# Kernel optimization log

Hardware: AMD Instinct MI355X
Metric: run time of the kernel (lower is better)

## Reference

```python
import jax, jax.numpy as jnp
import numpy as np
import math

NFFT = 2048; HOP = 512; BINS = NFFT // 2 + 1  # 1025
HEADS = 2; D = 2 * BINS; DFF = 4 * D          # 2050, 8200
BATCH = 4; LEN = 441000


def _stft(x, window):
    # replicates torch.stft(center=True, pad_mode='reflect', onesided=True)
    pad = NFFT // 2
    xp = jnp.pad(x, ((0, 0), (pad, pad)), mode='reflect')
    n_frames = 1 + (xp.shape[-1] - NFFT) // HOP
    idx = jnp.arange(n_frames)[:, None] * HOP + jnp.arange(NFFT)[None, :]
    frames = xp[:, idx] * window                      # (N, T, NFFT)
    return jnp.fft.rfft(frames, axis=-1).transpose(0, 2, 1)  # (N, BINS, T)


def _istft(spec, window, length):
    # replicates torch.istft(center=True, length=length)
    frames = jnp.fft.irfft(spec.transpose(0, 2, 1), n=NFFT, axis=-1) * window  # (N,T,NFFT)
    T = frames.shape[1]
    out_len = NFFT + HOP * (T - 1)
    idx = jnp.arange(T)[:, None] * HOP + jnp.arange(NFFT)[None, :]
    out = jnp.zeros((frames.shape[0], out_len), frames.dtype).at[:, idx].add(frames)
    wsq = jnp.zeros((out_len,), window.dtype).at[idx].add(window ** 2)
    out = out / jnp.where(wsq > 1e-11, wsq, 1.0)
    pad = NFFT // 2
    return out[:, pad:pad + length]


def _pos_enc(d, T):
    pos = jnp.arange(T, dtype=jnp.float32)[:, None]
    div = jnp.exp(jnp.arange(0, d, 2, dtype=jnp.float32) * (-math.log(10000.0) / d))
    pe = jnp.zeros((T, d), jnp.float32)
    pe = pe.at[:, 0::2].set(jnp.sin(pos * div)).at[:, 1::2].set(jnp.cos(pos * div))
    return pe[None]


def _ln(x, g, b):
    m = x.mean(-1, keepdims=True)
    v = x.var(-1, keepdims=True)
    return (x - m) / jnp.sqrt(v + 1e-5) * g + b


def _clin(r, i, Wr, br, Wi, bi):
    # (Lr(r) - Li(i), Lr(i) + Li(r))
    return (r @ Wr.T + br) - (i @ Wi.T + bi), (i @ Wr.T + br) + (r @ Wi.T + bi)


def _cconv1x1(r, i, wr, br, wi, bi):
    # 1x1 grouped conv with in=out=2, groups=2 -> per-channel scale+bias
    s = lambda x, w, b: x * w[None, :, None, None] + b[None, :, None, None]
    return s(r, wr, br) - s(i, wi, bi), s(i, wr, br) + s(r, wi, bi)


def _cattn(r, i, Win, bin_, Wo, bo):
    # 8 shared-weight MHA calls; only 4 distinct (Q,K) softmax maps, each
    # applied to two V tensors (the fusion opportunity). Eval mode: no dropout.
    B, S, _ = r.shape
    hd = D // HEADS
    Wq, Wk, Wv = Win[:D], Win[D:2 * D], Win[2 * D:]
    bq, bk, bv = bin_[:D], bin_[D:2 * D], bin_[2 * D:]
    proj = lambda x, W, b: (x @ W.T + b).reshape(B, S, HEADS, hd).transpose(0, 2, 1, 3)
    qr, qi = proj(r, Wq, bq), proj(i, Wq, bq)
    kr, ki = proj(r, Wk, bk), proj(i, Wk, bk)
    vr, vi = proj(r, Wv, bv), proj(i, Wv, bv)
    scale = 1.0 / math.sqrt(hd)
    A = lambda q, k: jax.nn.softmax(jnp.einsum('bhqd,bhkd->bhqk', q, k) * scale, axis=-1)
    Arr, Ari, Air, Aii = A(qr, kr), A(qr, ki), A(qi, kr), A(qi, ki)
    ap = lambda Aw, v: jnp.einsum('bhqk,bhkd->bhqd', Aw, v)
    out_r = ap(Arr, vr) + ap(Ari, vi) - ap(Air, vi) - ap(Aii, vr)
    out_i = ap(Arr, vi) + ap(Ari, vr) + ap(Air, vr) - ap(Aii, vi)
    merge = lambda o: o.transpose(0, 2, 1, 3).reshape(B, S, D)
    # out_proj bias coefficients: real part (+1+1-1-1)=0, imag part (+1+1+1-1)=2
    return merge(out_r) @ Wo.T, merge(out_i) @ Wo.T + 2.0 * bo


def reference(mix, window, c1wr, c1br, c1wi, c1bi, c2wr, c2br, c2wi, c2bi,
              attn_in_w, attn_in_b, attn_out_w, attn_out_b,
              l1wr, l1br, l1wi, l1bi, l2wr, l2br, l2wi, l2bi,
              n1_gr, n1_br, n1_gi, n1_bi, n2_gr, n2_br, n2_gi, n2_bi):
    B, C, L = mix.shape
    spec = _stft(mix.reshape(-1, L), window)      # (B*2, BINS, T)
    T = spec.shape[-1]
    spec = spec.reshape(-1, 2, BINS, T)           # (B, 2, BINS, T)
    real, imag = jnp.real(spec), jnp.imag(spec)
    nr, ni = _cconv1x1(real, imag, c1wr, c1br, c1wi, c1bi)
    nr = nr.transpose(0, 3, 2, 1).reshape(B, T, D)   # torch .transpose(1,3).reshape
    ni = ni.transpose(0, 3, 2, 1).reshape(B, T, D)
    pe = _pos_enc(D, T)
    nr, ni = nr + pe, ni + pe
    nr, ni = _cattn(nr, ni, attn_in_w, attn_in_b, attn_out_w, attn_out_b)
    nr, ni = _ln(nr, n1_gr, n1_br), _ln(ni, n1_gi, n1_bi)   # dropout = identity (eval)
    hr, hi = _clin(nr, ni, l1wr, l1br, l1wi, l1bi)
    hr, hi = jax.nn.relu(hr), jax.nn.relu(hi)
    hr, hi = _clin(hr, hi, l2wr, l2br, l2wi, l2bi)
    nr, ni = _ln(hr, n2_gr, n2_br), _ln(hi, n2_gi, n2_bi)
    nr = nr.reshape(B, T, BINS, 2).transpose(0, 3, 2, 1)    # (B,2,BINS,T)
    ni = ni.reshape(B, T, BINS, 2).transpose(0, 3, 2, 1)
    mr, mi = _cconv1x1(nr, ni, c2wr, c2br, c2wi, c2bi)
    real = real * jax.nn.sigmoid(mr)
    imag = imag * jax.nn.sigmoid(mi)
    spec2 = (real + 1j * imag).reshape(-1, BINS, T)
    estim = _istft(spec2, window, L).reshape(-1, 2, L)
    return estim, jnp.stack((jnp.real(spec2), jnp.imag(spec2)), axis=-1)


def setup_inputs() -> dict:
    key = jax.random.key(0)
    ks = jax.random.split(key, 32)
    W = 0.02
    rn = lambda k, shp, s=W: jax.random.normal(k, shp, jnp.float32) * s
    hann = 0.5 * (1.0 - jnp.cos(2.0 * jnp.pi * jnp.arange(NFFT, dtype=jnp.float32) / NFFT))
    inp = {
        'mix': rn(ks[0], (BATCH, 2, LEN), 1.0),
        'window': hann,
        'c1wr': rn(ks[1], (2,), 0.5), 'c1br': rn(ks[2], (2,), 0.1),
        'c1wi': rn(ks[3], (2,), 0.5), 'c1bi': rn(ks[4], (2,), 0.1),
        'c2wr': rn(ks[5], (2,), 0.5), 'c2br': rn(ks[6], (2,), 0.1),
        'c2wi': rn(ks[7], (2,), 0.5), 'c2bi': rn(ks[8], (2,), 0.1),
        'attn_in_w': rn(ks[9], (3 * D, D)), 'attn_in_b': rn(ks[10], (3 * D,)),
        'attn_out_w': rn(ks[11], (D, D)), 'attn_out_b': rn(ks[12], (D,)),
        'l1wr': rn(ks[13], (DFF, D)), 'l1br': rn(ks[14], (DFF,)),
        'l1wi': rn(ks[15], (DFF, D)), 'l1bi': rn(ks[16], (DFF,)),
        'l2wr': rn(ks[17], (D, DFF)), 'l2br': rn(ks[18], (D,)),
        'l2wi': rn(ks[19], (D, DFF)), 'l2bi': rn(ks[20], (D,)),
        'n1_gr': jnp.ones((D,), jnp.float32), 'n1_br': jnp.zeros((D,), jnp.float32),
        'n1_gi': jnp.ones((D,), jnp.float32), 'n1_bi': jnp.zeros((D,), jnp.float32),
        'n2_gr': jnp.ones((D,), jnp.float32), 'n2_br': jnp.zeros((D,), jnp.float32),
        'n2_gi': jnp.ones((D,), jnp.float32), 'n2_bi': jnp.zeros((D,), jnp.float32),
    }
    return inp
```

## Files before the change

### kernel.cpp

```cpp
#include <hip/hip_runtime.h>
#include <hip/hip_bf16.h>
#include <math.h>

#ifndef M_PIf
#define M_PIf 3.14159265358979323846f
#endif

static constexpr int kNFFT = 2048;
static constexpr int kHOP  = 512;
static constexpr int kBINS = 1025;
static constexpr int kT    = 862;
static constexpr int kL    = 441000;
static constexpr int kB    = 4;
static constexpr int kNSIG = 8;
static constexpr int kD    = 2050;
static constexpr int kHD   = 1025;
static constexpr int kDFF  = 8200;
static constexpr int kBS   = kB * kT;
static constexpr float kAttnScale = 0.031234752377721214f;
static constexpr long kS2  = (long)kT * kT;
static constexpr int kTP   = 864;
static constexpr long kS2P = (long)kT * kTP;
static constexpr int kDP   = 2056;
static constexpr int kHDP  = 1032;
static constexpr int kHDP2 = 1056;
static constexpr int kQKr  = 3488;
static constexpr int kWr   = 1152;
static constexpr int kNH   = 4104;
static constexpr int kDP2  = 2080;
static constexpr int kNHP  = 4128;
static constexpr int kMP   = 3456;
static constexpr int kW1R  = 4352;
static constexpr int kW2R  = 2304;

using bf16 = __hip_bfloat16;
typedef __attribute__((ext_vector_type(4))) float f32x4;
typedef __attribute__((ext_vector_type(8))) short bf16x8;

__device__ __forceinline__ float ldf(const float* p, long i) { return p[i]; }
__device__ __forceinline__ float ldf(const bf16* p, long i) {
  return __bfloat162float(p[i]);
}
__device__ __forceinline__ void sto(float* p, long i, float v) { p[i] = v; }
__device__ __forceinline__ void sto(bf16* p, long i, float v) {
  p[i] = __float2bfloat16(v);
}
__device__ __forceinline__ void load16(const float* src, bf16* dst) {
#pragma unroll
  for (int e = 0; e < 16; ++e) dst[e] = __float2bfloat16(src[e]);
}
__device__ __forceinline__ void load16(const bf16* src, bf16* dst) {
  *(bf16x8*)(dst)     = *(const bf16x8*)(src);
  *(bf16x8*)(dst + 8) = *(const bf16x8*)(src + 8);
}

__device__ __forceinline__ void glds16(const bf16* g, bf16* l) {
  __builtin_amdgcn_global_load_lds(
      (const __attribute__((address_space(1))) unsigned int*)g,
      (__attribute__((address_space(3))) unsigned int*)l, 16, 0, 0);
}

__device__ __forceinline__ void xcd_swizzle(int& bx, int& by) {
  int nwg = gridDim.x * gridDim.y;
  int orig = by * gridDim.x + bx;
  int qq = nwg >> 3, rr = nwg & 7;
  int xcd = orig & 7, loc = orig >> 3;
  int wg = (xcd < rr ? xcd * (qq + 1) : rr * (qq + 1) + (xcd - rr) * qq) + loc;
  bx = wg % gridDim.x;
  by = wg / gridDim.x;
}

__device__ __forceinline__ void pipe_wait8() {
  asm volatile("s_waitcnt vmcnt(8)" ::: "memory");
  __builtin_amdgcn_sched_barrier(0);
  __builtin_amdgcn_s_barrier();
  __builtin_amdgcn_sched_barrier(0);
}
__device__ __forceinline__ void pipe_wait0() {
  asm volatile("s_waitcnt vmcnt(0)" ::: "memory");
  __builtin_amdgcn_sched_barrier(0);
  __builtin_amdgcn_s_barrier();
  __builtin_amdgcn_sched_barrier(0);
}
__device__ __forceinline__ void pipe_readdone() {
  __builtin_amdgcn_sched_barrier(0);
  __builtin_amdgcn_s_barrier();
  __builtin_amdgcn_sched_barrier(0);
}

template <typename T>
__device__ __forceinline__ void stage_row16(const T* S, int grow, int glim,
                                            int lda, int k0sk, int K,
                                            bf16* dst) {
  bf16 tmp[16];
  if (grow < glim && k0sk + 16 <= K) {
    load16(S + (long)grow * lda + k0sk, tmp);
  } else {
#pragma unroll
    for (int e = 0; e < 16; ++e) {
      int gk = k0sk + e;
      tmp[e] = __float2bfloat16(
          (grow < glim && gk < K) ? ldf(S, (long)grow * lda + gk) : 0.f);
    }
  }
  *(bf16x8*)(dst)     = *(bf16x8*)&tmp[0];
  *(bf16x8*)(dst + 8) = *(bf16x8*)&tmp[8];
}

__global__ void k_twiddle(float2* __restrict__ tw) {
  int m = blockIdx.x * 256 + threadIdx.x;
  if (m < 1024) {
    float s, c;
    sincosf(M_PIf * (float)m / 1024.f, &s, &c);
    tw[m] = make_float2(c, s);
  }
}

__device__ __forceinline__ void fft2048_lds(float*& sr, float*& si,
                                            float* dr, float* di, int tid,
                                            float dir,
                                            const float2* __restrict__ tw) {
  int s = 0;
  for (int Ns = 1; Ns < 2048; Ns <<= 1, ++s) {
#pragma unroll
    for (int q = 0; q < 4; ++q) {
      int j = tid + q * 256;
      int base = j & (Ns - 1);
      int grp = j >> s;
      float2 t = tw[base << (10 - s)];
      float c = t.x, sn = dir * t.y;
      float ar = sr[j],        ai = si[j];
      float br = sr[j + 1024], bi = si[j + 1024];
      float tbr = br * c - bi * sn;
      float tbi = br * sn + bi * c;
      int o = (grp << (s + 1)) + base;
      dr[o]      = ar + tbr;  di[o]      = ai + tbi;
      dr[o + Ns] = ar - tbr;  di[o + Ns] = ai - tbi;
    }
    __syncthreads();
    float* t0 = sr; sr = dr; dr = t0;
    float* t1 = si; si = di; di = t1;
  }
}

__global__ __launch_bounds__(256) void k_stft(const float* __restrict__ mix,
                                              const float* __restrict__ win,
                                              const float2* __restrict__ tw,
                                              float* __restrict__ spec) {
  __shared__ float b0r[2048], b0i[2048], b1r[2048], b1i[2048];
  int t = blockIdx.x, sig = blockIdx.y, tid = threadIdx.x;
  const float* x = mix + (long)sig * kL;
  for (int i = tid; i < 2048; i += 256) {
    int src = t * kHOP + i - 1024;
    if (src < 0) src = -src;
    if (src >= kL) src = 2 * kL - 2 - src;
    b0r[i] = x[src] * win[i];
    b0i[i] = 0.f;
  }
  __syncthreads();
  float* sr = b0r; float* si = b0i;
  fft2048_lds(sr, si, b1r, b1i, tid, -1.f, tw);
  for (int k = tid; k < kBINS; k += 256) {
    long o = ((long)sig * kBINS + k) * kT + t;
    spec[o * 2]     = sr[k];
    spec[o * 2 + 1] = si[k];
  }
}

__global__ __launch_bounds__(256) void k_istft(const float* __restrict__ spec,
                                               const float* __restrict__ win,
// ... 13 lines not shown
  }
  __syncthreads();
  float* sr = b0r; float* si = b0i;
  fft2048_lds(sr, si, b1r, b1i, tid, +1.f, tw);
  const float scale = 1.f / 2048.f;
  float* fo = frames + ((long)sig * kT + t) * 2048;
  for (int n = tid; n < 2048; n += 256) fo[n] = sr[n] * scale * win[n];
}

__global__ void k_gather(const float* __restrict__ frames,
                         const float* __restrict__ win,
                         float* __restrict__ out0) {
  long idx = (long)blockIdx.x * 256 + threadIdx.x;
  long total = (long)kNSIG * kL;
  if (idx >= total) return;
  int sig = (int)(idx / kL);
  int l = (int)(idx % kL);
  int j = l + 1024;
  int tmax = j >> 9; if (tmax > kT - 1) tmax = kT - 1;
  int v = j - 1536;
  int tmin = v > 0 ? (v >> 9) : 0;
  float acc = 0.f, w2 = 0.f;
  for (int t = tmin; t <= tmax; ++t) {
    int n = j - (t << 9);
    float w = win[n];
    acc += frames[((long)sig * kT + t) * 2048 + n];
    w2 = fmaf(w, w, w2);
  }
  out0[idx] = acc / (w2 > 1e-11f ? w2 : 1.f);
}

__global__ void k_conv1_pe(const float* __restrict__ spec,
                           const float* __restrict__ c1wr, const float* __restrict__ c1br,
                           const float* __restrict__ c1wi, const float* __restrict__ c1bi,
                           bf16* __restrict__ xrh, bf16* __restrict__ xrl,
                           bf16* __restrict__ xih, bf16* __restrict__ xil) {
  long idx = (long)blockIdx.x * 256 + threadIdx.x;
  long total = (long)kB * 2 * kBINS * kT;
  if (idx >= total) return;
  int t = (int)(idx % kT);
  long r0 = idx / kT;
  int bin = (int)(r0 % kBINS);
  long r1 = r0 / kBINS;
  int ch = (int)(r1 % 2);
  int b = (int)(r1 / 2);
  float re = spec[idx * 2], im = spec[idx * 2 + 1];
  float wr = c1wr[ch], br = c1br[ch], wi = c1wi[ch], bi = c1bi[ch];
  float nr = (re * wr + br) - (im * wi + bi);
  float ni = (im * wr + br) + (re * wi + bi);
  int d = bin * 2 + ch;
  int k = d >> 1;
  float dv = expf((float)k * (-9.210340371976184f / 1025.0f));
  float arg = (float)t * dv;
  float pe = (d & 1) ? cosf(arg) : sinf(arg);
  long ro = ((long)(b * kT + t)) * kDP2 + d;
  float vr = nr + pe, vi = ni + pe;
  bf16 hr = __float2bfloat16(vr);
  bf16 hi = __float2bfloat16(vi);
  xrh[ro] = hr; xrl[ro] = __float2bfloat16(vr - __bfloat162float(hr));
  xih[ro] = hi; xil[ro] = __float2bfloat16(vi - __bfloat162float(hi));
}

__global__ void k_cvt2(const float* __restrict__ src, bf16* __restrict__ dst,
                       long total, int ldd, int srows, int scols, int lds) {
  long idx = (long)blockIdx.x * 256 + threadIdx.x;
  if (idx >= total) return;
  int r = (int)(idx / ldd), c = (int)(idx % ldd);
  float v = (r < srows && c < scols) ? src[(long)r * lds + c] : 0.f;
  dst[idx] = __float2bfloat16(v);
}

__global__ void k_cvt2s(const float* __restrict__ src, bf16* __restrict__ dh,
                        bf16* __restrict__ dl, long total, int ldd, int srows,
                        int scols, int lds) {
  long idx = (long)blockIdx.x * 256 + threadIdx.x;
  if (idx >= total) return;
  int r = (int)(idx / ldd), c = (int)(idx % ldd);
  float v = (r < srows && c < scols) ? src[(long)r * lds + c] : 0.f;
  bf16 h = __float2bfloat16(v);
  dh[idx] = h;
  dl[idx] = __float2bfloat16(v - __bfloat162float(h));
}

template <typename TA, typename TC>
__global__ __launch_bounds__(256) void k_mfma2(
    const TA* __restrict__ A1, const TA* __restrict__ A2,
    const bf16* __restrict__ B, TC* __restrict__ C1, TC* __restrict__ C2,
    const float* __restrict__ bias, float bs1, float bs2,
    int M, int N, int K, int lda, int ldb, int ldc) {
  __shared__ __align__(16) bf16 As1[128][40];
  __shared__ __align__(16) bf16 As2[128][40];
  __shared__ __align__(16) bf16 Bs[128][40];
  int tid = threadIdx.x;
  int bm = blockIdx.y * 128, bn = blockIdx.x * 128;
  int lane = tid & 63, w = tid >> 6;
  int wr = (w >> 1) * 64, wc = (w & 1) * 64;
  int fr = lane & 15, fq = lane >> 4;
  f32x4 ac1[4][4] = {}, ac2[4][4] = {};
  int sr = tid >> 1, sk = (tid & 1) * 16;
  for (int k0 = 0; k0 < K; k0 += 32) {
    stage_row16(A1, bm + sr, M, lda, k0 + sk, K, &As1[sr][sk]);
    stage_row16(A2, bm + sr, M, lda, k0 + sk, K, &As2[sr][sk]);
    stage_row16(B,  bn + sr, N, ldb, k0 + sk, K, &Bs[sr][sk]);
    __syncthreads();
    bf16x8 a1[4], a2[4], b[4];
#pragma unroll
    for (int i = 0; i < 4; ++i) {
      a1[i] = *(const bf16x8*)&As1[wr + i * 16 + fr][fq * 8];
      a2[i] = *(const bf16x8*)&As2[wr + i * 16 + fr][fq * 8];
      b[i]  = *(const bf16x8*)&Bs[wc + i * 16 + fr][fq * 8];
    }
#pragma unroll
    for (int i = 0; i < 4; ++i)
#pragma unroll
      for (int j = 0; j < 4; ++j) {
        ac1[i][j] = __builtin_amdgcn_mfma_f32_16x16x32_bf16(a1[i], b[j], ac1[i][j], 0, 0, 0);
        ac2[i][j] = __builtin_amdgcn_mfma_f32_16x16x32_bf16(a2[i], b[j], ac2[i][j], 0, 0, 0);
      }
    __syncthreads();
  }
#pragma unroll
  for (int i = 0; i < 4; ++i)
#pragma unroll
    for (int j = 0; j < 4; ++j) {
      int gn = bn + wc + j * 16 + fr;
      if (gn >= N) continue;
      float bv = bias ? bias[gn] : 0.f;
#pragma unroll
      for (int r = 0; r < 4; ++r) {
        int gm = bm + wr + i * 16 + fq * 4 + r;
        if (gm >= M) continue;
        long co = (long)gm * ldc + gn;
        sto(C1, co, ac1[i][j][r] + bs1 * bv);
        sto(C2, co, ac2[i][j][r] + bs2 * bv);
      }
    }
}

__global__ __launch_bounds__(256) void k_gemm3s(
    const bf16* __restrict__ Ah, const bf16* __restrict__ Al,
    const bf16* __restrict__ Bh, const bf16* __restrict__ Bl,
    bf16* __restrict__ Ch, bf16* __restrict__ Cl,
    const float* __restrict__ bias,
    int M, int N, int K, int lda, int ldb, int ldc) {
  __shared__ __align__(16) bf16 Sah[2][128][32];
  __shared__ __align__(16) bf16 Sal[2][128][32];
  __shared__ __align__(16) bf16 Sbh[2][128][32];
  __shared__ __align__(16) bf16 Sbl[2][128][32];
  int bx = blockIdx.x, by = blockIdx.y;
  xcd_swizzle(bx, by);
  int bm = by * 128, bn = bx * 128;
  int tid = threadIdx.x;
  int lane = tid & 63, w = tid >> 6;
  int wr = (w >> 1) * 64, wc = (w & 1) * 64;
  int fr = lane & 15, fq = lane >> 4;
  f32x4 acc[4][4] = {};
  int srow = w * 32 + (lane >> 2);
  int scol = (lane & 3) * 8;
  const bf16* pAh[2]; const bf16* pAl[2];
  const bf16* pBh[2]; const bf16* pBl[2];
#pragma unroll
  for (int c = 0; c < 2; ++c) {
    long ga = (long)(bm + srow + c * 16) * lda + scol;
    long gb = (long)(bn + srow + c * 16) * ldb + scol;
    pAh[c] = Ah + ga; pAl[c] = Al + ga;
    pBh[c] = Bh + gb; pBl[c] = Bl + gb;
  }
  int nt = K >> 5;
#pragma unroll
  for (int c = 0; c < 2; ++c) {
    int lb = w * 1024 + c * 512;
    glds16(pAh[c], &Sah[0][0][0] + lb);
    glds16(pAl[c], &Sal[0][0][0] + lb);
    glds16(pBh[c], &Sbh[0][0][0] + lb);
    glds16(pBl[c], &Sbl[0][0][0] + lb);
  }
  if (nt > 1) {
#pragma unroll
    for (int c = 0; c < 2; ++c) {
      int lb = 4096 + w * 1024 + c * 512;
      glds16(pAh[c] + 32, &Sah[0][0][0] + lb);
      glds16(pAl[c] + 32, &Sal[0][0][0] + lb);
      glds16(pBh[c] + 32, &Sbh[0][0][0] + lb);
      glds16(pBl[c] + 32, &Sbl[0][0][0] + lb);
    }
  }
  long koff = 64;
  for (int t = 0; t < nt; ++t) {
    int p = t & 1;
    if (t + 1 < nt) pipe_wait8(); else pipe_wait0();
    bf16x8 ah[4], al[4], bh[4], bl[4];
#pragma unroll
    for (int i = 0; i < 4; ++i) {
      ah[i] = *(const bf16x8*)&Sah[p][wr + i * 16 + fr][fq * 8];
      al[i] = *(const bf16x8*)&Sal[p][wr + i * 16 + fr][fq * 8];
      bh[i] = *(const bf16x8*)&Sbh[p][wc + i * 16 + fr][fq * 8];
      bl[i] = *(const bf16x8*)&Sbl[p][wc + i * 16 + fr][fq * 8];
    }
#pragma unroll
    for (int i = 0; i < 4; ++i)
#pragma unroll
      for (int j = 0; j < 4; ++j) {
        acc[i][j] = __builtin_amdgcn_mfma_f32_16x16x32_bf16(ah[i], bh[j], acc[i][j], 0, 0, 0);
        acc[i][j] = __builtin_amdgcn_mfma_f32_16x16x32_bf16(ah[i], bl[j], acc[i][j], 0, 0, 0);
        acc[i][j] = __builtin_amdgcn_mfma_f32_16x16x32_bf16(al[i], bh[j], acc[i][j], 0, 0, 0);
      }
    pipe_readdone();
    if (t + 2 < nt) {
      int pb = p * 4096;
#pragma unroll
      for (int c = 0; c < 2; ++c) {
        int lb = pb + w * 1024 + c * 512;
        glds16(pAh[c] + koff, &Sah[0][0][0] + lb);
        glds16(pAl[c] + koff, &Sal[0][0][0] + lb);
        glds16(pBh[c] + koff, &Sbh[0][0][0] + lb);
        glds16(pBl[c] + koff, &Sbl[0][0][0] + lb);
      }
      koff += 32;
    }
  }
#pragma unroll
  for (int i = 0; i < 4; ++i)
#pragma unroll
    for (int j = 0; j < 4; ++j) {
      int gn = bn + wc + j * 16 + fr;
      if (gn >= N) continue;
      float bv = bias[gn];
#pragma unroll
      for (int r = 0; r < 4; ++r) {
        int gm = bm + wr + i * 16 + fq * 4 + r;
        if (gm >= M) continue;
        long co = (long)gm * ldc + gn;
        float v = acc[i][j][r] + bv;
        bf16 h = __float2bfloat16(v);
        Ch[co] = h;
        Cl[co] = __float2bfloat16(v - __bfloat162float(h));
      }
    }
}

__global__ __launch_bounds__(256) void k_qkt3(
    const bf16* __restrict__ Qrh, const bf16* __restrict__ Qrl,
    const bf16* __restrict__ Qih, const bf16* __restrict__ Qil,
    const bf16* __restrict__ Krh, const bf16* __restrict__ Krl,
    const bf16* __restrict__ Kih, const bf16* __restrict__ Kil,
    float* __restrict__ S, int bp) {
  __shared__ __align__(16) bf16 Sqh[2][128][32];
  __shared__ __align__(16) bf16 Sql[2][128][32];
  __shared__ __align__(16) bf16 Skh[2][128][32];
  __shared__ __align__(16) bf16 Skl[2][128][32];
  int bl = blockIdx.z >> 2, c = blockIdx.z & 3;
  int b = bp * 2 + bl;
  long roff = (long)b * kT * kHDP2;
  const bf16* qh = ((c >> 1) ? Qih : Qrh) + roff;
  const bf16* ql = ((c >> 1) ? Qil : Qrl) + roff;
  const bf16* kh = ((c & 1) ? Kih : Krh) + roff;
  const bf16* kl = ((c & 1) ? Kil : Krl) + roff;
  float* So = S + ((long)bl * 4 + c) * kS2;
  int bx = blockIdx.x, by = blockIdx.y;
  xcd_swizzle(bx, by);
  int bm = by * 128, bn = bx * 128;
  int tid = threadIdx.x;
  int lane = tid & 63, w = tid >> 6;
  int wr = (w >> 1) * 64, wc = (w & 1) * 64;
  int fr = lane & 15, fq = lane >> 4;
  f32x4 acc[4][4] = {};
  int srow = w * 32 + (lane >> 2);
  int scol = (lane & 3) * 8;
  const bf16* pQh[2]; const bf16* pQl[2];
  const bf16* pKh[2]; const bf16* pKl[2];
#pragma unroll
  for (int cc = 0; cc < 2; ++cc) {
    long ga = (long)(bm + srow + cc * 16) * kHDP2 + scol;
    long gb = (long)(bn + srow + cc * 16) * kHDP2 + scol;
    pQh[cc] = qh + ga; pQl[cc] = ql + ga;
    pKh[cc] = kh + gb; pKl[cc] = kl + gb;
  }
  int nt = kHDP2 >> 5;
#pragma unroll
  for (int cc = 0; cc < 2; ++cc) {
    int lb = w * 1024 + cc * 512;
    glds16(pQh[cc], &Sqh[0][0][0] + lb);
    glds16(pQl[cc], &Sql[0][0][0] + lb);
    glds16(pKh[cc], &Skh[0][0][0] + lb);
    glds16(pKl[cc], &Skl[0][0][0] + lb);
  }
  if (nt > 1) {
#pragma unroll
    for (int cc = 0; cc < 2; ++cc) {
      int lb = 4096 + w * 1024 + cc * 512;
      glds16(pQh[cc] + 32, &Sqh[0][0][0] + lb);
      glds16(pQl[cc] + 32, &Sql[0][0][0] + lb);
      glds16(pKh[cc] + 32, &Skh[0][0][0] + lb);
      glds16(pKl[cc] + 32, &Skl[0][0][0] + lb);
    }
  }
  long koff = 64;
  for (int t = 0; t < nt; ++t) {
    int p = t & 1;
    if (t + 1 < nt) pipe_wait8(); else pipe_wait0();
    bf16x8 ah[4], al[4], bh[4], blv[4];
#pragma unroll
    for (int i = 0; i < 4; ++i) {
      ah[i]  = *(const bf16x8*)&Sqh[p][wr + i * 16 + fr][fq * 8];
      al[i]  = *(const bf16x8*)&Sql[p][wr + i * 16 + fr][fq * 8];
      bh[i]  = *(const bf16x8*)&Skh[p][wc + i * 16 + fr][fq * 8];
      blv[i] = *(const bf16x8*)&Skl[p][wc + i * 16 + fr][fq * 8];
    }
#pragma unroll
    for (int i = 0; i < 4; ++i)
#pragma unroll
      for (int j = 0; j < 4; ++j) {
        acc[i][j] = __builtin_amdgcn_mfma_f32_16x16x32_bf16(ah[i], bh[j],  acc[i][j], 0, 0, 0);
        acc[i][j] = __builtin_amdgcn_mfma_f32_16x16x32_bf16(ah[i], blv[j], acc[i][j], 0, 0, 0);
        acc[i][j] = __builtin_amdgcn_mfma_f32_16x16x32_bf16(al[i], bh[j],  acc[i][j], 0, 0, 0);
      }
    pipe_readdone();
    if (t + 2 < nt) {
      int pb = p * 4096;
#pragma unroll
      for (int cc = 0; cc < 2; ++cc) {
        int lb = pb + w * 1024 + cc * 512;
        glds16(pQh[cc] + koff, &Sqh[0][0][0] + lb);
        glds16(pQl[cc] + koff, &Sql[0][0][0] + lb);
        glds16(pKh[cc] + koff, &Skh[0][0][0] + lb);
        glds16(pKl[cc] + koff, &Skl[0][0][0] + lb);
      }
      koff += 32;
    }
  }
#pragma unroll
  for (int i = 0; i < 4; ++i)
#pragma unroll
    for (int j = 0; j < 4; ++j) {
      int gn = bn + wc + j * 16 + fr;
      if (gn >= kT) continue;
#pragma unroll
      for (int r = 0; r < 4; ++r) {
        int gm = bm + wr + i * 16 + fq * 4 + r;
        if (gm >= kT) continue;
        So[(long)gm * kT + gn] = acc[i][j][r];
      }
    }
}

template <typename TC>
__global__ __launch_bounds__(512) void k_cgemm(
    const bf16* __restrict__ Ar, const bf16* __restrict__ Ai,
    const bf16* __restrict__ Br, const bf16* __restrict__ Bi,
    TC* __restrict__ Cr, TC* __restrict__ Ci,
    const float* __restrict__ biasR, const float* __restrict__ biasI,
    float bscale, int accum, int relu, int Nreal,
    int M, int N, int K, int lda, int ldb, int ldc) {
  __shared__ __align__(16) bf16 Asr[128][32];
  __shared__ __align__(16) bf16 Asi[128][32];
  __shared__ __align__(16) bf16 Bsr[256][32];
  __shared__ __align__(16) bf16 Bsi[256][32];
  int bx = blockIdx.x, by = blockIdx.y;
  xcd_swizzle(bx, by);
  int bm = by * 128, bn = bx * 256;
  int tid = threadIdx.x;
  int lane = tid & 63, w = tid >> 6;
  int wr = (w >> 2) * 64, wc = (w & 3) * 64;
  int fr = lane & 15, fq = lane >> 4;
  f32x4 acR[4][4] = {}, acI[4][4] = {};
  int srow = w * 16 + (lane >> 2);
  int scol = (lane & 3) * 8;
  const bf16* pAr = Ar + (long)(bm + srow) * lda + scol;
  const bf16* pAi = Ai + (long)(bm + srow) * lda + scol;
  const bf16* pBr[2];
  const bf16* pBi[2];
#pragma unroll
  for (int c = 0; c < 2; ++c) {
    long gb = (long)(bn + c * 128 + srow) * ldb + scol;
    pBr[c] = Br + gb;
    pBi[c] = Bi + gb;
  }
  const short ks = (short)0x8000;
  const bf16x8 sgn = {ks, ks, ks, ks, ks, ks, ks, ks};
  for (int k0 = 0; k0 < K; k0 += 32) {
    glds16(pAr + k0, &Asr[0][0] + w * 512);
    glds16(pAi + k0, &Asi[0][0] + w * 512);
#pragma unroll
    for (int c = 0; c < 2; ++c) {
      int lb = c * 4096 + w * 512;
      glds16(pBr[c] + k0, &Bsr[0][0] + lb);
      glds16(pBi[c] + k0, &Bsi[0][0] + lb);
    }
    __syncthreads();
    bf16x8 ar[4], ai[4], nai[4];
#pragma unroll
    for (int i = 0; i < 4; ++i) {
      ar[i] = *(const bf16x8*)&Asr[wr + i * 16 + fr][fq * 8];
      ai[i] = *(const bf16x8*)&Asi[wr + i * 16 + fr][fq * 8];
      nai[i] = ai[i] ^ sgn;
    }
#pragma unroll
    for (int j = 0; j < 4; ++j) {
      bf16x8 br = *(const bf16x8*)&Bsr[wc + j * 16 + fr][fq * 8];
      bf16x8 bi = *(const bf16x8*)&Bsi[wc + j * 16 + fr][fq * 8];
#pragma unroll
      for (int i = 0; i < 4; ++i) {
        acR[i][j] = __builtin_amdgcn_mfma_f32_16x16x32_bf16(ar[i],  br, acR[i][j], 0, 0, 0);
        acR[i][j] = __builtin_amdgcn_mfma_f32_16x16x32_bf16(nai[i], bi, acR[i][j], 0, 0, 0);
        acI[i][j] = __builtin_amdgcn_mfma_f32_16x16x32_bf16(ai[i],  br, acI[i][j], 0, 0, 0);
        acI[i][j] = __builtin_amdgcn_mfma_f32_16x16x32_bf16(ar[i],  bi, acI[i][j], 0, 0, 0);
      }
    }
    __syncthreads();
  }
#pragma unroll
  for (int i = 0; i < 4; ++i)
// ... 173 lines not shown
  float* x = X + row * d;
  int tid = threadIdx.x;
  float s = 0.f, s2 = 0.f;
  for (int i = tid; i < d; i += 256) {
    float v = x[i];
    s += v;
    s2 = fmaf(v, v, s2);
  }
  __shared__ float rs[4], rs2[4];
  for (int o = 32; o > 0; o >>= 1) {
    s += __shfl_down(s, o);
    s2 += __shfl_down(s2, o);
  }
  int lane = tid & 63, w = tid >> 6;
  if (lane == 0) { rs[w] = s; rs2[w] = s2; }
  __syncthreads();
  float st = rs[0] + rs[1] + rs[2] + rs[3];
  float s2t = rs2[0] + rs2[1] + rs2[2] + rs2[3];
  float m = st / d;
  float var = s2t / d - m * m;
  float inv = rsqrtf(var + 1e-5f);
  for (int i = tid; i < d; i += 256) x[i] = (x[i] - m) * inv * g[i] + b[i];
}

__global__ void k_mask(const float* __restrict__ gr_, const float* __restrict__ gi_,
                       const float* __restrict__ c2wr, const float* __restrict__ c2br,
                       const float* __restrict__ c2wi, const float* __restrict__ c2bi,
                       float* __restrict__ spec) {
  long idx = (long)blockIdx.x * 256 + threadIdx.x;
  long total = (long)kB * 2 * kBINS * kT;
  if (idx >= total) return;
  int t = (int)(idx % kT);
  long r0 = idx / kT;
  int bin = (int)(r0 % kBINS);
  long r1 = r0 / kBINS;
  int ch = (int)(r1 % 2);
  int b = (int)(r1 / 2);
  long ro = ((long)(b * kT + t)) * kD + (bin * 2 + ch);
  float gr = gr_[ro], gi = gi_[ro];
  float wr = c2wr[ch], br = c2br[ch], wi = c2wi[ch], bi = c2bi[ch];
  float mr = (gr * wr + br) - (gi * wi + bi);
  float mi = (gi * wr + br) + (gr * wi + bi);
  float re = spec[idx * 2], im = spec[idx * 2 + 1];
  spec[idx * 2]     = re / (1.f + expf(-mr));
  spec[idx * 2 + 1] = im / (1.f + expf(-mi));
}

extern "C" void kernel_launch(void* const* d_in, const int* in_sizes, int n_in,
                              void* d_out, int out_size, void* d_ws, size_t ws_size,
                              hipStream_t stream) {
  const float* mix        = (const float*)d_in[0];
  const float* window     = (const float*)d_in[1];
  const float* c1wr       = (const float*)d_in[2];
  const float* c1br       = (const float*)d_in[3];
  const float* c1wi       = (const float*)d_in[4];
  const float* c1bi       = (const float*)d_in[5];
  const float* c2wr       = (const float*)d_in[6];
  const float* c2br       = (const float*)d_in[7];
  const float* c2wi       = (const float*)d_in[8];
  const float* c2bi       = (const float*)d_in[9];
  const float* attn_in_w  = (const float*)d_in[10];
  const float* attn_in_b  = (const float*)d_in[11];
  const float* attn_out_w = (const float*)d_in[12];
  const float* attn_out_b = (const float*)d_in[13];
  const float* l1wr       = (const float*)d_in[14];
  const float* l1br       = (const float*)d_in[15];
  const float* l1wi       = (const float*)d_in[16];
  const float* l1bi       = (const float*)d_in[17];
  const float* l2wr       = (const float*)d_in[18];
  const float* l2br       = (const float*)d_in[19];
  const float* l2wi       = (const float*)d_in[20];
  const float* l2bi       = (const float*)d_in[21];
  const float* n1_gr      = (const float*)d_in[22];
  const float* n1_br      = (const float*)d_in[23];
  const float* n1_gi      = (const float*)d_in[24];
  const float* n1_bi      = (const float*)d_in[25];
  const float* n2_gr      = (const float*)d_in[26];
  const float* n2_br      = (const float*)d_in[27];
  const float* n2_gi      = (const float*)d_in[28];
  const float* n2_bi      = (const float*)d_in[29];

  constexpr long eX    = (long)kMP * kDP2;
  constexpr long eQK2  = (long)kQKr * kHDP2;
  constexpr long eAout = (long)kBS * kDP;
  constexpr long eV    = (long)kBS * kHDP;
  constexpr long eWp   = (long)kWr * kDP2;
  constexpr long eHidp = (long)kMP * kNHP;
  constexpr long eW1p  = (long)kW1R * kDP2;
  constexpr long eW2p  = (long)kW2R * kNHP;

  constexpr size_t oX    = 0;
  constexpr size_t oQK   = oX + 4 * eX * 2;
  constexpr size_t oAout = oQK + 8 * eQK2 * 2;
  constexpr size_t oV    = oAout + 2 * eAout * 2;
  constexpr size_t oW    = oV + 2 * eV * 2;
  constexpr size_t oP    = oW + 5 * eWp * 2;
  constexpr size_t oTW   = oP + 3 * kS2P * 2;
  constexpr size_t kNeed = 188922816;
  static_assert(oTW + 8192 <= kNeed, "tw overflow");
  constexpr size_t oSS = oW;
  static_assert(oSS + 8 * kS2 * 4 <= oP, "sS overflow");
  static_assert(2 * (long)kBS * kD * 4 <= (long)oQK, "xr/xi overlay");
  static_assert((long)kD * kDP * 2 <= (long)(oW - oV), "Wob overlay");
  constexpr size_t oAb  = oQK;
  constexpr size_t oWF  = oAb + 2 * eX * 2;
  constexpr size_t oHid = oWF + 2 * eW2p * 2;
  static_assert(2 * eW1p * 2 <= 2 * eW2p * 2, "W slot sized by W2");
  static_assert(oHid + 2 * eHidp * 2 <= oTW, "hid overflow");
  static_assert((long)kNSIG * kT * 2048 * 4 <= (long)(oTW - oAb), "frames");

  char* wsb = (char*)d_ws;
  if (ws_size < kNeed) return;

  bf16*  Xrh = (bf16*)(wsb + oX);
  bf16*  Xrl = Xrh + eX;
  bf16*  Xih = Xrl + eX;
  bf16*  Xil = Xih + eX;
  bf16*  Qrh = (bf16*)(wsb + oQK);
  bf16*  Qrl = Qrh + eQK2;
  bf16*  Qih = Qrl + eQK2;
  bf16*  Qil = Qih + eQK2;
  bf16*  Krh = Qil + eQK2;
  bf16*  Krl = Krh + eQK2;
  bf16*  Kih = Krl + eQK2;
  bf16*  Kil = Kih + eQK2;
  bf16*  aoutR = (bf16*)(wsb + oAout);
  bf16*  aoutI = aoutR + eAout;
  bf16*  Vr = (bf16*)(wsb + oV);
  bf16*  Vi = Vr + eV;
  bf16*  Wqh = (bf16*)(wsb + oW);
  bf16*  Wql = Wqh + eWp;
  bf16*  Wkh = Wql + eWp;
  bf16*  Wkl = Wkh + eWp;
  bf16*  Wvh = Wkl + eWp;
  float* sS = (float*)(wsb + oSS);
  bf16*  Pbuf = (bf16*)(wsb + oP);
  bf16*  Wob = (bf16*)(wsb + oV);
  float* xr = (float*)(wsb + oX);
  float* xi = xr + (long)kBS * kD;
  bf16*  AbR = (bf16*)(wsb + oAb);
  bf16*  AbI = AbR + eX;
  bf16*  w1rH = (bf16*)(wsb + oWF);
  bf16*  w1iH = w1rH + eW1p;
  bf16*  w2rH = (bf16*)(wsb + oWF);
  bf16*  w2iH = w2rH + eW2p;
  bf16*  hidR = (bf16*)(wsb + oHid);
  bf16*  hidI = hidR + eHidp;
  float* frames = (float*)(wsb + oAb);
  float2* tw = (float2*)(wsb + oTW);

  float* out0 = (float*)d_out;
  float* spec = out0 + (long)kNSIG * kL;

  auto cvt2 = [&](const float* src, bf16* dst, int dstRows, int ldd,
                  int srows, int scols, int lds) {
    long total = (long)dstRows * ldd;
    k_cvt2<<<(int)((total + 255) / 256), 256, 0, stream>>>(src, dst, total,
                                                           ldd, srows, scols,
                                                           lds);
  };
  auto cvt2s = [&](const float* src, bf16* dh, bf16* dl, int dstRows, int ldd,
                   int srows, int scols, int lds) {
    long total = (long)dstRows * ldd;
    k_cvt2s<<<(int)((total + 255) / 256), 256, 0, stream>>>(
        src, dh, dl, total, ldd, srows, scols, lds);
  };

  hipMemsetAsync(d_ws, 0, kNeed, stream);
  k_twiddle<<<4, 256, 0, stream>>>(tw);

  k_stft<<<dim3(kT, kNSIG), 256, 0, stream>>>(mix, window, tw, spec);

  long nct = (long)kB * 2 * kBINS * kT;
  k_conv1_pe<<<(nct + 255) / 256, 256, 0, stream>>>(spec, c1wr, c1br, c1wi,
                                                    c1bi, Xrh, Xrl, Xih, Xil);

  for (int h = 0; h < 2; ++h) {
    const float* Wq = attn_in_w + (long)(h * kHD) * kD;
    const float* Wk = attn_in_w + (long)(kD + h * kHD) * kD;
    const float* Wv = attn_in_w + (long)(2 * kD + h * kHD) * kD;
    const float* bq = attn_in_b + h * kHD;
    const float* bk = attn_in_b + kD + h * kHD;
    const float* bv = attn_in_b + 2 * kD + h * kHD;
    cvt2s(Wq, Wqh, Wql, kWr, kDP2, kHD, kD, kD);
    cvt2s(Wk, Wkh, Wkl, kWr, kDP2, kHD, kD, kD);
    cvt2(Wv, Wvh, kWr, kDP2, kHD, kD, kD);
    k_mfma2<bf16, bf16><<<dim3(9, 27), 256, 0, stream>>>(
        Xrh, Xih, Wvh, Vr, Vi, bv, 1.f, 1.f, kBS, kHD, kD, kDP2, kDP2, kHDP);
    k_gemm3s<<<dim3(9, 27), 256, 0, stream>>>(
        Xrh, Xrl, Wqh, Wql, Qrh, Qrl, bq, kBS, kHD, kDP2, kDP2, kDP2, kHDP2);
    k_gemm3s<<<dim3(9, 27), 256, 0, stream>>>(
        Xih, Xil, Wqh, Wql, Qih, Qil, bq, kBS, kHD, kDP2, kDP2, kDP2, kHDP2);
    k_gemm3s<<<dim3(9, 27), 256, 0, stream>>>(
        Xrh, Xrl, Wkh, Wkl, Krh, Krl, bk, kBS, kHD, kDP2, kDP2, kDP2, kHDP2);
    k_gemm3s<<<dim3(9, 27), 256, 0, stream>>>(
        Xih, Xil, Wkh, Wkl, Kih, Kil, bk, kBS, kHD, kDP2, kDP2, kDP2, kHDP2);
    for (int bp = 0; bp < 2; ++bp) {
      k_qkt3<<<dim3(7, 7, 8), 256, 0, stream>>>(Qrh, Qrl, Qih, Qil,
                                                Krh, Krl, Kih, Kil, sS, bp);
      for (int bl = 0; bl < 2; ++bl) {
        int b = bp * 2 + bl;
        k_smf<<<kT, 256, 0, stream>>>(sS + (long)bl * 4 * kS2, Pbuf);
        k_pv<<<dim3(9, 7), 256, 0, stream>>>(
            Pbuf, Vr + (long)b * kT * kHDP, Vi + (long)b * kT * kHDP,
            aoutR + (long)b * kT * kDP + h * kHD,
            aoutI + (long)b * kT * kDP + h * kHD,
            kT, kHD, kT, kTP, kHDP, kDP);
      }
    }
  }

  cvt2(attn_out_w, Wob, kD, kDP, kD, kD, kD);
  k_mfma2<bf16, float><<<dim3(17, 27), 256, 0, stream>>>(
      aoutR, aoutI, Wob, xr, xi, attn_out_b, 0.f, 2.f,
      kBS, kD, kD, kDP, kDP, kD);

  k_ln<<<kBS, 256, 0, stream>>>(xr, n1_gr, n1_br, kD);
  k_ln<<<kBS, 256, 0, stream>>>(xi, n1_gi, n1_bi, kD);

  cvt2(xr, AbR, kMP, kDP2, kBS, kD, kD);
  cvt2(xi, AbI, kMP, kDP2, kBS, kD, kD);
  for (int nh = 0; nh < 2; ++nh) {
    int srows = (nh ? kDFF - kNH : kNH);
    cvt2(l1wr + (long)nh * kNH * kD, w1rH, kW1R, kDP2, srows, kD, kD);
    cvt2(l1wi + (long)nh * kNH * kD, w1iH, kW1R, kDP2, srows, kD, kD);
    k_cgemm<bf16><<<dim3(17, 27), 512, 0, stream>>>(
        AbR, AbI, w1rH, w1iH, hidR, hidI,
        l1br + nh * kNH, l1bi + nh * kNH, 1.f, 0, 1, srows,
        kBS, kNHP, kDP2, kDP2, kDP2, kNHP);
    cvt2(l2wr + nh * kNH, w2rH, kW2R, kNHP, kD, srows, kDFF);
    cvt2(l2wi + nh * kNH, w2iH, kW2R, kNHP, kD, srows, kDFF);
    k_cgemm<float><<<dim3(9, 27), 512, 0, stream>>>(
        hidR, hidI, w2rH, w2iH, xr, xi,
        l2br, l2bi, (nh == 0 ? 1.f : 0.f), nh, 0, kD,
        kBS, kD, kNHP, kNHP, kNHP, kD);
  }

  k_ln<<<kBS, 256, 0, stream>>>(xr, n2_gr, n2_br, kD);
  k_ln<<<kBS, 256, 0, stream>>>(xi, n2_gi, n2_bi, kD);

  k_mask<<<(nct + 255) / 256, 256, 0, stream>>>(xr, xi, c2wr, c2br, c2wi,
                                                c2bi, spec);

  k_istft<<<dim3(kT, kNSIG), 256, 0, stream>>>(spec, window, tw, frames);
  k_gather<<<(int)(((long)kNSIG * kL + 255) / 256), 256, 0, stream>>>(
      frames, window, out0);
}
```

Baseline: 4.941 ms.

## Enlarge GEMM tiles to 256x128 with 8 waves and direct-to-LDS loads

The Q/K/V projection, QK^T and output-projection GEMMs move from 128x128 tiles with 4 waves to 256x128 tiles with 8 waves. This cuts redundant global traffic for the B operand and launches fewer, larger workgroups. The V and output-projection GEMM now stage operands with global_load_lds and XCD swizzling instead of per-thread register staging, and the attention output buffers are padded to kDP2 so K is tile-aligned. In exchange, the explicit double-buffered pipeline in the split-bf16 kernels is dropped for a simple single-buffer loop with two barriers, which can expose load latency. The larger M tiles also read unguarded rows past the padded row counts.

```diff
diff --git a/kernel.cpp b/kernel.cpp
--- a/kernel.cpp
+++ b/kernel.cpp
@@ -21,11 +21,11 @@
 static constexpr long kS2  = (long)kT * kT;
 static constexpr int kTP   = 864;
 static constexpr long kS2P = (long)kT * kTP;
-static constexpr int kDP   = 2056;
 static constexpr int kHDP  = 1032;
 static constexpr int kHDP2 = 1056;
 static constexpr int kQKr  = 3488;
 static constexpr int kWr   = 1152;
+static constexpr int kWoR  = 2176;
 static constexpr int kNH   = 4104;
 static constexpr int kDP2  = 2080;
 static constexpr int kNHP  = 4128;
@@ -68,24 +68,6 @@
   int wg = (xcd < rr ? xcd * (qq + 1) : rr * (qq + 1) + (xcd - rr) * qq) + loc;
   bx = wg % gridDim.x;
   by = wg / gridDim.x;
-}
-
-__device__ __forceinline__ void pipe_wait8() {
-  asm volatile("s_waitcnt vmcnt(8)" ::: "memory");
-  __builtin_amdgcn_sched_barrier(0);
-  __builtin_amdgcn_s_barrier();
-  __builtin_amdgcn_sched_barrier(0);
-}
-__device__ __forceinline__ void pipe_wait0() {
-  asm volatile("s_waitcnt vmcnt(0)" ::: "memory");
-  __builtin_amdgcn_sched_barrier(0);
-  __builtin_amdgcn_s_barrier();
-  __builtin_amdgcn_sched_barrier(0);
-}
-__device__ __forceinline__ void pipe_readdone() {
-  __builtin_amdgcn_sched_barrier(0);
-  __builtin_amdgcn_s_barrier();
-  __builtin_amdgcn_sched_barrier(0);
 }
 
 template <typename T>
@@ -265,26 +247,44 @@
   dl[idx] = __float2bfloat16(v - __bfloat162float(h));
 }
 
-template <typename TA, typename TC>
-__global__ __launch_bounds__(256) void k_mfma2(
-    const TA* __restrict__ A1, const TA* __restrict__ A2,
+
+template <typename TC>
+__global__ __launch_bounds__(512) void k_mfma2g(
+    const bf16* __restrict__ A1, const bf16* __restrict__ A2,
     const bf16* __restrict__ B, TC* __restrict__ C1, TC* __restrict__ C2,
     const float* __restrict__ bias, float bs1, float bs2,
     int M, int N, int K, int lda, int ldb, int ldc) {
-  __shared__ __align__(16) bf16 As1[128][40];
-  __shared__ __align__(16) bf16 As2[128][40];
-  __shared__ __align__(16) bf16 Bs[128][40];
+  __shared__ __align__(16) bf16 As1[256][32];
+  __shared__ __align__(16) bf16 As2[256][32];
+  __shared__ __align__(16) bf16 Bs[128][32];
+  int bx = blockIdx.x, by = blockIdx.y;
+  xcd_swizzle(bx, by);
+  int bm = by * 256, bn = bx * 128;
   int tid = threadIdx.x;
-  int bm = blockIdx.y * 128, bn = blockIdx.x * 128;
   int lane = tid & 63, w = tid >> 6;
   int wr = (w >> 1) * 64, wc = (w & 1) * 64;
   int fr = lane & 15, fq = lane >> 4;
   f32x4 ac1[4][4] = {}, ac2[4][4] = {};
-  int sr = tid >> 1, sk = (tid & 1) * 16;
+  int srA = w * 32 + (lane >> 2);
+  int srB = w * 16 + (lane >> 2);
+  int scol = (lane & 3) * 8;
+  const bf16* pA1[2];
+  const bf16* pA2[2];
+#pragma unroll
+  for (int c = 0; c < 2; ++c) {
+    long ga = (long)(bm + srA + c * 16) * lda + scol;
+    pA1[c] = A1 + ga;
+    pA2[c] = A2 + ga;
+  }
+  const bf16* pB = B + (long)(bn + srB) * ldb + scol;
   for (int k0 = 0; k0 < K; k0 += 32) {
-    stage_row16(A1, bm + sr, M, lda, k0 + sk, K, &As1[sr][sk]);
-    stage_row16(A2, bm + sr, M, lda, k0 + sk, K, &As2[sr][sk]);
-    stage_row16(B,  bn + sr, N, ldb, k0 + sk, K, &Bs[sr][sk]);
+#pragma unroll
+    for (int c = 0; c < 2; ++c) {
+      int lb = w * 1024 + c * 512;
+      glds16(pA1[c] + k0, &As1[0][0] + lb);
+      glds16(pA2[c] + k0, &As2[0][0] + lb);
+    }
+    glds16(pB + k0, &Bs[0][0] + w * 512);
     __syncthreads();
     bf16x8 a1[4], a2[4], b[4];
 #pragma unroll
@@ -320,65 +320,55 @@
     }
 }
 
-__global__ __launch_bounds__(256) void k_gemm3s(
+__global__ __launch_bounds__(512) void k_gemm3s8(
     const bf16* __restrict__ Ah, const bf16* __restrict__ Al,
     const bf16* __restrict__ Bh, const bf16* __restrict__ Bl,
     bf16* __restrict__ Ch, bf16* __restrict__ Cl,
     const float* __restrict__ bias,
     int M, int N, int K, int lda, int ldb, int ldc) {
-  __shared__ __align__(16) bf16 Sah[2][128][32];
-  __shared__ __align__(16) bf16 Sal[2][128][32];
-  __shared__ __align__(16) bf16 Sbh[2][128][32];
-  __shared__ __align__(16) bf16 Sbl[2][128][32];
+  __shared__ __align__(16) bf16 Sah[256][32];
+  __shared__ __align__(16) bf16 Sal[256][32];
+  __shared__ __align__(16) bf16 Sbh[128][32];
+  __shared__ __align__(16) bf16 Sbl[128][32];
   int bx = blockIdx.x, by = blockIdx.y;
   xcd_swizzle(bx, by);
-  int bm = by * 128, bn = bx * 128;
+  int bm = by * 256, bn = bx * 128;
   int tid = threadIdx.x;
   int lane = tid & 63, w = tid >> 6;
   int wr = (w >> 1) * 64, wc = (w & 1) * 64;
   int fr = lane & 15, fq = lane >> 4;
   f32x4 acc[4][4] = {};
-  int srow = w * 32 + (lane >> 2);
+  int srA = w * 32 + (lane >> 2);
+  int srB = w * 16 + (lane >> 2);
   int scol = (lane & 3) * 8;
-  const bf16* pAh[2]; const bf16* pAl[2];
-  const bf16* pBh[2]; const bf16* pBl[2];
+  const bf16* pAh[2];
+  const bf16* pAl[2];
 #pragma unroll
   for (int c = 0; c < 2; ++c) {
-    long ga = (long)(bm + srow + c * 16) * lda + scol;
-    long gb = (long)(bn + srow + c * 16) * ldb + scol;
-    pAh[c] = Ah + ga; pAl[c] = Al + ga;
-    pBh[c] = Bh + gb; pBl[c] = Bl + gb;
-  }
-  int nt = K >> 5;
-#pragma unroll
-  for (int c = 0; c < 2; ++c) {
-    int lb = w * 1024 + c * 512;
-    glds16(pAh[c], &Sah[0][0][0] + lb);
-    glds16(pAl[c], &Sal[0][0][0] + lb);
-    glds16(pBh[c], &Sbh[0][0][0] + lb);
-    glds16(pBl[c], &Sbl[0][0][0] + lb);
-  }
-  if (nt > 1) {
+    long ga = (long)(bm + srA + c * 16) * lda + scol;
+    pAh[c] = Ah + ga;
+    pAl[c] = Al + ga;
+  }
+  long gb = (long)(bn + srB) * ldb + scol;
+  const bf16* pBh = Bh + gb;
+  const bf16* pBl = Bl + gb;
+  for (int k0 = 0; k0 < K; k0 += 32) {
 #pragma unroll
     for (int c = 0; c < 2; ++c) {
-      int lb = 4096 + w * 1024 + c * 512;
-      glds16(pAh[c] + 32, &Sah[0][0][0] + lb);
-      glds16(pAl[c] + 32, &Sal[0][0][0] + lb);
-      glds16(pBh[c] + 32, &Sbh[0][0][0] + lb);
-      glds16(pBl[c] + 32, &Sbl[0][0][0] + lb);
-    }
-  }
-  long koff = 64;
-  for (int t = 0; t < nt; ++t) {
-    int p = t & 1;
-    if (t + 1 < nt) pipe_wait8(); else pipe_wait0();
+      int lb = w * 1024 + c * 512;
+      glds16(pAh[c] + k0, &Sah[0][0] + lb);
+      glds16(pAl[c] + k0, &Sal[0][0] + lb);
+    }
+    glds16(pBh + k0, &Sbh[0][0] + w * 512);
+    glds16(pBl + k0, &Sbl[0][0] + w * 512);
+    __syncthreads();
     bf16x8 ah[4], al[4], bh[4], bl[4];
 #pragma unroll
     for (int i = 0; i < 4; ++i) {
-      ah[i] = *(const bf16x8*)&Sah[p][wr + i * 16 + fr][fq * 8];
-      al[i] = *(const bf16x8*)&Sal[p][wr + i * 16 + fr][fq * 8];
-      bh[i] = *(const bf16x8*)&Sbh[p][wc + i * 16 + fr][fq * 8];
-      bl[i] = *(const bf16x8*)&Sbl[p][wc + i * 16 + fr][fq * 8];
+      ah[i] = *(const bf16x8*)&Sah[wr + i * 16 + fr][fq * 8];
+      al[i] = *(const bf16x8*)&Sal[wr + i * 16 + fr][fq * 8];
+      bh[i] = *(const bf16x8*)&Sbh[wc + i * 16 + fr][fq * 8];
+      bl[i] = *(const bf16x8*)&Sbl[wc + i * 16 + fr][fq * 8];
     }
 #pragma unroll
     for (int i = 0; i < 4; ++i)
@@ -388,19 +378,7 @@
         acc[i][j] = __builtin_amdgcn_mfma_f32_16x16x32_bf16(ah[i], bl[j], acc[i][j], 0, 0, 0);
         acc[i][j] = __builtin_amdgcn_mfma_f32_16x16x32_bf16(al[i], bh[j], acc[i][j], 0, 0, 0);
       }
-    pipe_readdone();
-    if (t + 2 < nt) {
-      int pb = p * 4096;
-#pragma unroll
-      for (int c = 0; c < 2; ++c) {
-        int lb = pb + w * 1024 + c * 512;
-        glds16(pAh[c] + koff, &Sah[0][0][0] + lb);
-        glds16(pAl[c] + koff, &Sal[0][0][0] + lb);
-        glds16(pBh[c] + koff, &Sbh[0][0][0] + lb);
-        glds16(pBl[c] + koff, &Sbl[0][0][0] + lb);
-      }
-      koff += 32;
-    }
+    __syncthreads();
   }
 #pragma unroll
   for (int i = 0; i < 4; ++i)
@@ -422,16 +400,16 @@
     }
 }
 
-__global__ __launch_bounds__(256) void k_qkt3(
+__global__ __launch_bounds__(512) void k_qkt38(
     const bf16* __restrict__ Qrh, const bf16* __restrict__ Qrl,
     const bf16* __restrict__ Qih, const bf16* __restrict__ Qil,
     const bf16* __restrict__ Krh, const bf16* __restrict__ Krl,
     const bf16* __restrict__ Kih, const bf16* __restrict__ Kil,
     float* __restrict__ S, int bp) {
-  __shared__ __align__(16) bf16 Sqh[2][128][32];
-  __shared__ __align__(16) bf16 Sql[2][128][32];
-  __shared__ __align__(16) bf16 Skh[2][128][32];
-  __shared__ __align__(16) bf16 Skl[2][128][32];
+  __shared__ __align__(16) bf16 Sqh[256][32];
+  __shared__ __align__(16) bf16 Sql[256][32];
+  __shared__ __align__(16) bf16 Skh[128][32];
+  __shared__ __align__(16) bf16 Skl[128][32];
   int bl = blockIdx.z >> 2, c = blockIdx.z & 3;
   int b = bp * 2 + bl;
   long roff = (long)b * kT * kHDP2;
@@ -442,75 +420,53 @@
   float* So = S + ((long)bl * 4 + c) * kS2;
   int bx = blockIdx.x, by = blockIdx.y;
   xcd_swizzle(bx, by);
-  int bm = by * 128, bn = bx * 128;
+  int bm = by * 256, bn = bx * 128;
   int tid = threadIdx.x;
   int lane = tid & 63, w = tid >> 6;
   int wr = (w >> 1) * 64, wc = (w & 1) * 64;
   int fr = lane & 15, fq = lane >> 4;
   f32x4 acc[4][4] = {};
-  int srow = w * 32 + (lane >> 2);
+  int srA = w * 32 + (lane >> 2);
+  int srB = w * 16 + (lane >> 2);
   int scol = (lane & 3) * 8;
-  const bf16* pQh[2]; const bf16* pQl[2];
-  const bf16* pKh[2]; const bf16* pKl[2];
+  const bf16* pQh[2];
+  const bf16* pQl[2];
 #pragma unroll
   for (int cc = 0; cc < 2; ++cc) {
-    long ga = (long)(bm + srow + cc * 16) * kHDP2 + scol;
-    long gb = (long)(bn + srow + cc * 16) * kHDP2 + scol;
-    pQh[cc] = qh + ga; pQl[cc] = ql + ga;
-    pKh[cc] = kh + gb; pKl[cc] = kl + gb;
-  }
-  int nt = kHDP2 >> 5;
-#pragma unroll
-  for (int cc = 0; cc < 2; ++cc) {
-    int lb = w * 1024 + cc * 512;
-    glds16(pQh[cc], &Sqh[0][0][0] + lb);
-    glds16(pQl[cc], &Sql[0][0][0] + lb);
-    glds16(pKh[cc], &Skh[0][0][0] + lb);
-    glds16(pKl[cc], &Skl[0][0][0] + lb);
-  }
-  if (nt > 1) {
+    long ga = (long)(bm + srA + cc * 16) * kHDP2 + scol;
+    pQh[cc] = qh + ga;
+    pQl[cc] = ql + ga;
+  }
+  long gb = (long)(bn + srB) * kHDP2 + scol;
+  const bf16* pKh = kh + gb;
+  const bf16* pKl = kl + gb;
+  for (int k0 = 0; k0 < kHDP2; k0 += 32) {
 #pragma unroll
     for (int cc = 0; cc < 2; ++cc) {
-      int lb = 4096 + w * 1024 + cc * 512;
-      glds16(pQh[cc] + 32, &Sqh[0][0][0] + lb);
-      glds16(pQl[cc] + 32, &Sql[0][0][0] + lb);
-      glds16(pKh[cc] + 32, &Skh[0][0][0] + lb);
-      glds16(pKl[cc] + 32, &Skl[0][0][0] + lb);
-    }
-  }
-  long koff = 64;
-  for (int t = 0; t < nt; ++t) {
-    int p = t & 1;
-    if (t + 1 < nt) pipe_wait8(); else pipe_wait0();
-    bf16x8 ah[4], al[4], bh[4], blv[4];
+      int lb = w * 1024 + cc * 512;
+      glds16(pQh[cc] + k0, &Sqh[0][0] + lb);
+      glds16(pQl[cc] + k0, &Sql[0][0] + lb);
+    }
+    glds16(pKh + k0, &Skh[0][0] + w * 512);
+    glds16(pKl + k0, &Skl[0][0] + w * 512);
+    __syncthreads();
+    bf16x8 ah[4], al[4], bh[4], bl[4];
 #pragma unroll
     for (int i = 0; i < 4; ++i) {
-      ah[i]  = *(const bf16x8*)&Sqh[p][wr + i * 16 + fr][fq * 8];
-      al[i]  = *(const bf16x8*)&Sql[p][wr + i * 16 + fr][fq * 8];
-      bh[i]  = *(const bf16x8*)&Skh[p][wc + i * 16 + fr][fq * 8];
-      blv[i] = *(const bf16x8*)&Skl[p][wc + i * 16 + fr][fq * 8];
+      ah[i] = *(const bf16x8*)&Sqh[wr + i * 16 + fr][fq * 8];
+      al[i] = *(const bf16x8*)&Sql[wr + i * 16 + fr][fq * 8];
+      bh[i] = *(const bf16x8*)&Skh[wc + i * 16 + fr][fq * 8];
+      bl[i] = *(const bf16x8*)&Skl[wc + i * 16 + fr][fq * 8];
     }
 #pragma unroll
     for (int i = 0; i < 4; ++i)
 #pragma unroll
       for (int j = 0; j < 4; ++j) {
-        acc[i][j] = __builtin_amdgcn_mfma_f32_16x16x32_bf16(ah[i], bh[j],  acc[i][j], 0, 0, 0);
-        acc[i][j] = __builtin_amdgcn_mfma_f32_16x16x32_bf16(ah[i], blv[j], acc[i][j], 0, 0, 0);
-        acc[i][j] = __builtin_amdgcn_mfma_f32_16x16x32_bf16(al[i], bh[j],  acc[i][j], 0, 0, 0);
-      }
-    pipe_readdone();
-    if (t + 2 < nt) {
-      int pb = p * 4096;
-#pragma unroll
-      for (int cc = 0; cc < 2; ++cc) {
-        int lb = pb + w * 1024 + cc * 512;
-        glds16(pQh[cc] + koff, &Sqh[0][0][0] + lb);
-        glds16(pQl[cc] + koff, &Sql[0][0][0] + lb);
-        glds16(pKh[cc] + koff, &Skh[0][0][0] + lb);
-        glds16(pKl[cc] + koff, &Skl[0][0][0] + lb);
-      }
-      koff += 32;
-    }
+        acc[i][j] = __builtin_amdgcn_mfma_f32_16x16x32_bf16(ah[i], bh[j], acc[i][j], 0, 0, 0);
+        acc[i][j] = __builtin_amdgcn_mfma_f32_16x16x32_bf16(ah[i], bl[j], acc[i][j], 0, 0, 0);
+        acc[i][j] = __builtin_amdgcn_mfma_f32_16x16x32_bf16(al[i], bh[j], acc[i][j], 0, 0, 0);
+      }
+    __syncthreads();
   }
 #pragma unroll
   for (int i = 0; i < 4; ++i)
@@ -850,7 +806,7 @@
 
   constexpr long eX    = (long)kMP * kDP2;
   constexpr long eQK2  = (long)kQKr * kHDP2;
-  constexpr long eAout = (long)kBS * kDP;
+  constexpr long eAout = (long)kBS * kDP2;
   constexpr long eV    = (long)kBS * kHDP;
   constexpr long eWp   = (long)kWr * kDP2;
   constexpr long eHidp = (long)kMP * kNHP;
@@ -864,12 +820,12 @@
   constexpr size_t oW    = oV + 2 * eV * 2;
   constexpr size_t oP    = oW + 5 * eWp * 2;
   constexpr size_t oTW   = oP + 3 * kS2P * 2;
-  constexpr size_t kNeed = 188922816;
-  static_assert(oTW + 8192 <= kNeed, "tw overflow");
+  constexpr size_t kNeed = oTW + 8192;
+  static_assert(kNeed <= 188922816, "ws ceiling");
   constexpr size_t oSS = oW;
   static_assert(oSS + 8 * kS2 * 4 <= oP, "sS overflow");
   static_assert(2 * (long)kBS * kD * 4 <= (long)oQK, "xr/xi overlay");
-  static_assert((long)kD * kDP * 2 <= (long)(oW - oV), "Wob overlay");
+  static_assert((long)kWoR * kDP2 * 2 <= (long)(oW - oV), "Wob overlay");
   constexpr size_t oAb  = oQK;
   constexpr size_t oWF  = oAb + 2 * eX * 2;
   constexpr size_t oHid = oWF + 2 * eW2p * 2;
@@ -953,35 +909,35 @@
     cvt2s(Wq, Wqh, Wql, kWr, kDP2, kHD, kD, kD);
     cvt2s(Wk, Wkh, Wkl, kWr, kDP2, kHD, kD, kD);
     cvt2(Wv, Wvh, kWr, kDP2, kHD, kD, kD);
-    k_mfma2<bf16, bf16><<<dim3(9, 27), 256, 0, stream>>>(
-        Xrh, Xih, Wvh, Vr, Vi, bv, 1.f, 1.f, kBS, kHD, kD, kDP2, kDP2, kHDP);
-    k_gemm3s<<<dim3(9, 27), 256, 0, stream>>>(
+    k_mfma2g<bf16><<<dim3(9, 14), 512, 0, stream>>>(
+        Xrh, Xih, Wvh, Vr, Vi, bv, 1.f, 1.f, kBS, kHD, kDP2, kDP2, kDP2, kHDP);
+    k_gemm3s8<<<dim3(9, 14), 512, 0, stream>>>(
         Xrh, Xrl, Wqh, Wql, Qrh, Qrl, bq, kBS, kHD, kDP2, kDP2, kDP2, kHDP2);
-    k_gemm3s<<<dim3(9, 27), 256, 0, stream>>>(
+    k_gemm3s8<<<dim3(9, 14), 512, 0, stream>>>(
         Xih, Xil, Wqh, Wql, Qih, Qil, bq, kBS, kHD, kDP2, kDP2, kDP2, kHDP2);
-    k_gemm3s<<<dim3(9, 27), 256, 0, stream>>>(
+    k_gemm3s8<<<dim3(9, 14), 512, 0, stream>>>(
         Xrh, Xrl, Wkh, Wkl, Krh, Krl, bk, kBS, kHD, kDP2, kDP2, kDP2, kHDP2);
-    k_gemm3s<<<dim3(9, 27), 256, 0, stream>>>(
+    k_gemm3s8<<<dim3(9, 14), 512, 0, stream>>>(
         Xih, Xil, Wkh, Wkl, Kih, Kil, bk, kBS, kHD, kDP2, kDP2, kDP2, kHDP2);
     for (int bp = 0; bp < 2; ++bp) {
-      k_qkt3<<<dim3(7, 7, 8), 256, 0, stream>>>(Qrh, Qrl, Qih, Qil,
-                                                Krh, Krl, Kih, Kil, sS, bp);
+      k_qkt38<<<dim3(7, 4, 8), 512, 0, stream>>>(Qrh, Qrl, Qih, Qil,
+                                                 Krh, Krl, Kih, Kil, sS, bp);
       for (int bl = 0; bl < 2; ++bl) {
         int b = bp * 2 + bl;
         k_smf<<<kT, 256, 0, stream>>>(sS + (long)bl * 4 * kS2, Pbuf);
         k_pv<<<dim3(9, 7), 256, 0, stream>>>(
             Pbuf, Vr + (long)b * kT * kHDP, Vi + (long)b * kT * kHDP,
-            aoutR + (long)b * kT * kDP + h * kHD,
-            aoutI + (long)b * kT * kDP + h * kHD,
-            kT, kHD, kT, kTP, kHDP, kDP);
-      }
-    }
-  }
-
-  cvt2(attn_out_w, Wob, kD, kDP, kD, kD, kD);
-  k_mfma2<bf16, float><<<dim3(17, 27), 256, 0, stream>>>(
+            aoutR + (long)b * kT * kDP2 + h * kHD,
+            aoutI + (long)b * kT * kDP2 + h * kHD,
+            kT, kHD, kT, kTP, kHDP, kDP2);
+      }
+    }
+  }
+
+  cvt2(attn_out_w, Wob, kWoR, kDP2, kD, kD, kD);
+  k_mfma2g<float><<<dim3(17, 14), 512, 0, stream>>>(
       aoutR, aoutI, Wob, xr, xi, attn_out_b, 0.f, 2.f,
-      kBS, kD, kD, kDP, kDP, kD);
+      kBS, kD, kDP2, kDP2, kDP2, kD);
 
   k_ln<<<kBS, 256, 0, stream>>>(xr, n1_gr, n1_br, kD);
   k_ln<<<kBS, 256, 0, stream>>>(xi, n1_gi, n1_bi, kD);
```

After: 5.138 ms. 1.04x slower.
